# Performance work log

Hardware: AMD Instinct MI355X
Metric: run time of the kernel (lower is better)

Reference implementation:

```python
import jax, jax.numpy as jnp
from jax import lax
import numpy as np

OBJECT_W, BCE_W, DICE_W = 2.0, 5.0, 5.0
B, N, M, C = 8, 128, 32, 65536


def setup_inputs() -> dict:
    key = jax.random.key(0)
    k1, k2, k3 = jax.random.split(key, 3)
    objectness = jax.random.normal(k1, (B, N), jnp.float32)
    pred_masks = jax.random.normal(k2, (B, N, C), jnp.float32)
    gt_masks = jax.random.randint(k3, (B, M, C), 0, 2).astype(jnp.float32)
    return {"objectness": objectness, "pred_masks": pred_masks, "gt_masks": gt_masks}


def _cost_matrices(objectness, pred, gt):
    # BCE-with-logits vs all-ones target: log(1+exp(-x)) = softplus(-x)
    # BCE-with-logits vs all-zeros target: softplus(x)
    sp_pos = jax.nn.softplus(-pred)                       # [B,N,C]
    sp_neg = jax.nn.softplus(pred)                        # [B,N,C]
    # einsum('nc,mc->nm', pos, t) + einsum('nc,mc->nm', neg, 1-t), batched.
    # neg @ (1-t) = neg.sum(c) - neg @ t (avoids materializing 1-t).
    bce = (jnp.einsum('bnc,bmc->bnm', sp_pos, gt)
           + sp_neg.sum(-1)[:, :, None]
           - jnp.einsum('bnc,bmc->bnm', sp_neg, gt)) / pred.shape[-1]
    s = jax.nn.sigmoid(pred)
    numerator = 2.0 * jnp.einsum('bnc,bmc->bnm', s, gt)
    denominator = s.sum(-1)[:, :, None] + gt.sum(-1)[:, None, :]
    dice = 1.0 - (numerator + 1.0) / (denominator + 1.0)
    obj = -jax.nn.sigmoid(objectness)[:, :, None]         # [B,N,1]
    return OBJECT_W * obj + BCE_W * bce + DICE_W * dice    # [B,N,M]


def _lsap(cost):
    """Jonker-Volgenant shortest-augmenting-path LSAP (scipy algorithm).
    cost: [R, C] with R <= C. Returns col4row [R] int32: column per row."""
    R, Cn = cost.shape
    BIG = jnp.float32(1e30)

    def outer(cur_row, carry):
        u, v, row4col, col4row = carry
        shortest = jnp.full((Cn,), BIG, jnp.float32)
        path = jnp.full((Cn,), -1, jnp.int32)
        SR = jnp.zeros((R,), bool)
        SC = jnp.zeros((Cn,), bool)

        def sp_cond(s):
            return s[6] < 0

        def sp_body(s):
            i, shortest, path, SR, SC, minVal, sink = s
            SR = SR.at[i].set(True)
            d = minVal + cost[i] - u[i] - v
            better = (d < shortest) & (~SC)
            shortest = jnp.where(better, d, shortest)
            path = jnp.where(better, i, path)
            masked = jnp.where(SC, BIG, shortest)
            j = jnp.argmin(masked).astype(jnp.int32)
            minVal = masked[j]
            SC = SC.at[j].set(True)
            nxt = row4col[j]
            sink = jnp.where(nxt == -1, j, jnp.int32(-1))
            i = jnp.where(nxt == -1, i, nxt)
            return (i, shortest, path, SR, SC, minVal, sink)

        init = (cur_row.astype(jnp.int32), shortest, path, SR, SC,
                jnp.float32(0.0), jnp.int32(-1))
        i, shortest, path, SR, SC, minVal, sink = lax.while_loop(sp_cond, sp_body, init)

        # dual updates (scipy rectangular_lsap)
        u = u.at[cur_row].add(minVal)
        extra = SR & (jnp.arange(R) != cur_row)
        sp_at_col = shortest[jnp.clip(col4row, 0, Cn - 1)]
        u = jnp.where(extra, u + minVal - sp_at_col, u)
        v = jnp.where(SC, v - (minVal - shortest), v)

        # augment along path
        def aug_cond(s):
            return ~s[3]

        def aug_body(s):
            j, row4col, col4row, done = s
            i = path[j]
            row4col = row4col.at[j].set(i)
            tmp = col4row[i]
            col4row = col4row.at[i].set(j)
            done = (i == cur_row)
            return (tmp, row4col, col4row, done)

        _, row4col, col4row, _ = lax.while_loop(
            aug_cond, aug_body, (sink, row4col, col4row, jnp.array(False)))
        return (u, v, row4col, col4row)

    carry = (jnp.zeros((R,), jnp.float32), jnp.zeros((Cn,), jnp.float32),
             jnp.full((Cn,), -1, jnp.int32), jnp.full((R,), -1, jnp.int32))
    u, v, row4col, col4row = lax.fori_loop(0, R, outer, carry)
    return col4row


def reference(objectness, pred_masks, gt_masks):
    cost = _cost_matrices(objectness, pred_masks, gt_masks)   # [B,N,M]
    # scipy lsap on [N,M] then sort by target == solving on cost.T [M,N]:
    # indices[b, m] = matched query index for target m.
    indices = jax.vmap(_lsap)(jnp.transpose(cost, (0, 2, 1)))  # [B,M]
    return cost, indices
```

## Files before the change

### kernel.cpp

```cpp
#include <hip/hip_runtime.h>
#include <hip/hip_bf16.h>

#define LOG2E 1.4426950408889634f
#define LN2   0.6931471805599453f

typedef __attribute__((ext_vector_type(8))) short short8;
typedef __attribute__((ext_vector_type(4))) float f32x4;

#define B_ 8
#define N_ 128
#define M_ 32
#define C_ 65536
#define KCHUNKS 64
#define KC (C_ / KCHUNKS)
#define BK 64
#define AST 72

__device__ __forceinline__ unsigned pack2(float lo, float hi) {
  union { __hip_bfloat16 h; unsigned short s; } a, b;
  a.h = __float2bfloat16(lo);
  b.h = __float2bfloat16(hi);
  return (unsigned)a.s | ((unsigned)b.s << 16);
}

__global__ __launch_bounds__(256, 2) void cost_partial_kernel(
    const float* __restrict__ pred, const float* __restrict__ gt,
    float* __restrict__ xg_part, float* __restrict__ sg_part,
    float* __restrict__ sp_part, float* __restrict__ ss_part,
    float* __restrict__ gts_part)
{
  __shared__ unsigned short As[256 * AST];
  __shared__ unsigned short Bt[32 * AST];
  const int kc = blockIdx.x, b = blockIdx.y;
  const int tid = threadIdx.x;
  const int grp = tid >> 4, gl = tid & 15;
  const int grow = tid >> 3, gh = tid & 7;
  const int wave = tid >> 6, lane = tid & 63;
  const int quad = lane >> 4, lcol = lane & 15;
  const int c0 = kc * KC;
  const int slab = kc * B_ + b;

  const float* predB = pred + (size_t)b * N_ * C_ + c0;
  const float* gtB   = gt   + (size_t)b * M_ * C_ + (size_t)grow * C_ + c0;

  float spr[8], sr[8], gtacc = 0.f;
#pragma unroll
  for (int r = 0; r < 8; ++r) { spr[r] = 0.f; sr[r] = 0.f; }

  f32x4 acc[4][2];
#pragma unroll
  for (int rt = 0; rt < 4; ++rt)
#pragma unroll
    for (int ct = 0; ct < 2; ++ct)
      acc[rt][ct] = (f32x4){0.f, 0.f, 0.f, 0.f};

  float4 p[8], g0, g1;
#pragma unroll
  for (int r = 0; r < 8; ++r)
    p[r] = *(const float4*)(predB + (size_t)(r * 16 + grp) * C_ + gl * 4);
  g0 = *(const float4*)(gtB + gh * 4);
  g1 = *(const float4*)(gtB + (gh + 8) * 4);

  for (int ks = 0; ks < KC / BK; ++ks) {
    float4 pn[8], gn0, gn1;
    if (ks + 1 < KC / BK) {
      const int cb = (ks + 1) * BK;
#pragma unroll
      for (int r = 0; r < 8; ++r)
        pn[r] = *(const float4*)(predB + (size_t)(r * 16 + grp) * C_ + cb + gl * 4);
      gn0 = *(const float4*)(gtB + cb + gh * 4);
      gn1 = *(const float4*)(gtB + cb + (gh + 8) * 4);
    }

#pragma unroll
    for (int r = 0; r < 8; ++r) {
      const int row = r * 16 + grp;
      float xs[4] = {p[r].x, p[r].y, p[r].z, p[r].w};
      float ss[4];
#pragma unroll
      for (int e = 0; e < 4; ++e) {
        float x = xs[e];
        float t = fminf(x * LOG2E, 80.f);
        float e2 = __builtin_amdgcn_exp2f(t);
        float z = 1.f + e2;
        float s = e2 * __builtin_amdgcn_rcpf(z);
        spr[r] += __builtin_amdgcn_logf(z);
        sr[r]  += s;
        ss[e] = s;
      }
      *(uint2*)&As[row * AST + gl * 4] =
          (uint2){pack2(xs[0], xs[1]), pack2(xs[2], xs[3])};
      *(uint2*)&As[(N_ + row) * AST + gl * 4] =
          (uint2){pack2(ss[0], ss[1]), pack2(ss[2], ss[3])};
    }
    gtacc += g0.x + g0.y + g0.z + g0.w + g1.x + g1.y + g1.z + g1.w;
    *(uint2*)&Bt[grow * AST + gh * 4] =
        (uint2){pack2(g0.x, g0.y), pack2(g0.z, g0.w)};
    *(uint2*)&Bt[grow * AST + (gh + 8) * 4] =
        (uint2){pack2(g1.x, g1.y), pack2(g1.z, g1.w)};
    __syncthreads();

#pragma unroll
    for (int k0 = 0; k0 < BK; k0 += 32) {
      const int koff = k0 + quad * 8;
      short8 bf0 = *(const short8*)&Bt[lcol * AST + koff];
      short8 bf1 = *(const short8*)&Bt[(16 + lcol) * AST + koff];
#pragma unroll
      for (int rt = 0; rt < 4; ++rt) {
        short8 af = *(const short8*)&As[(wave * 64 + rt * 16 + lcol) * AST + koff];
        acc[rt][0] = __builtin_amdgcn_mfma_f32_16x16x32_bf16(af, bf0, acc[rt][0], 0, 0, 0);
        acc[rt][1] = __builtin_amdgcn_mfma_f32_16x16x32_bf16(af, bf1, acc[rt][1], 0, 0, 0);
      }
    }
    __syncthreads();

    if (ks + 1 < KC / BK) {
#pragma unroll
      for (int r = 0; r < 8; ++r) p[r] = pn[r];
      g0 = gn0; g1 = gn1;
    }
  }

#pragma unroll
  for (int r = 0; r < 8; ++r) {
    float v1 = spr[r], v2 = sr[r];
#pragma unroll
    for (int off = 1; off < 16; off <<= 1) {
      v1 += __shfl_xor(v1, off);
      v2 += __shfl_xor(v2, off);
    }
    if (gl == 0) {
      sp_part[slab * N_ + r * 16 + grp] = v1 * LN2;
      ss_part[slab * N_ + r * 16 + grp] = v2;
    }
  }
  gtacc += __shfl_xor(gtacc, 1);
  gtacc += __shfl_xor(gtacc, 2);
  gtacc += __shfl_xor(gtacc, 4);
  if (gh == 0) gts_part[slab * M_ + grow] = gtacc;

#pragma unroll
  for (int rt = 0; rt < 4; ++rt)
#pragma unroll
    for (int ct = 0; ct < 2; ++ct)
#pragma unroll
      for (int reg = 0; reg < 4; ++reg) {
        int orow = wave * 64 + rt * 16 + quad * 4 + reg;
        int ocol = ct * 16 + lcol;
        float v = acc[rt][ct][reg];
        if (orow < N_) xg_part[(slab * N_ + orow) * M_ + ocol] = v;
        else           sg_part[(slab * N_ + (orow - N_)) * M_ + ocol] = v;
      }
}

__global__ void finalize_kernel(const float* __restrict__ obj,
    const float* __restrict__ xg_part, const float* __restrict__ sg_part,
    const float* __restrict__ sp_part, const float* __restrict__ ss_part,
    const float* __restrict__ gts_part, float* __restrict__ cost)
{
  int idx = blockIdx.x * blockDim.x + threadIdx.x;
  int b = idx >> 12;
  int n = (idx >> 5) & 127;
  int m = idx & 31;
  float xa = 0.f, sa = 0.f, spa = 0.f, ssa = 0.f, ga = 0.f;
#pragma unroll 4
  for (int kc = 0; kc < KCHUNKS; ++kc) {
    int slab = kc * B_ + b;
    xa  += xg_part[(slab * N_ + n) * M_ + m];
    sa  += sg_part[(slab * N_ + n) * M_ + m];
    spa += sp_part[slab * N_ + n];
    ssa += ss_part[slab * N_ + n];
    ga  += gts_part[slab * M_ + m];
  }
  float o = obj[b * N_ + n];
  float t = fminf(o * LOG2E, 80.f);
  float e2 = __builtin_amdgcn_exp2f(t);
  float sig = e2 * __builtin_amdgcn_rcpf(1.f + e2);
  float bce = (spa - xa) * (1.0f / (float)C_);
  float dice = 1.f - (2.f * sa + 1.f) / (ssa + ga + 1.f);
  cost[idx] = -2.f * sig + 5.f * bce + 5.f * dice;
}

#define BIGF 1e30f

__device__ __forceinline__ float wave_min_all(float x) {
  const int BI = __builtin_bit_cast(int, BIGF);
  int v = __builtin_bit_cast(int, x);
#define MIN_STEP(ctrl)                                                        \
  {                                                                           \
    int t_ = __builtin_amdgcn_update_dpp(BI, v, ctrl, 0xf, 0xf, false);       \
    v = __builtin_bit_cast(int, fminf(__builtin_bit_cast(float, v),           \
                                      __builtin_bit_cast(float, t_)));        \
  }
  MIN_STEP(0x111)
  MIN_STEP(0x112)
  MIN_STEP(0x114)
  MIN_STEP(0x118)
  MIN_STEP(0x142)
  MIN_STEP(0x143)
#undef MIN_STEP
  return __builtin_bit_cast(float, __builtin_amdgcn_readlane(v, 63));
}

__device__ __forceinline__ float rdlane_f(float x, int l) {
  return __builtin_bit_cast(float, __builtin_amdgcn_readlane(__builtin_bit_cast(int, x), l));
}

__global__ __launch_bounds__(64) void lsap_kernel(const float* __restrict__ cost,
                                                  float* __restrict__ out)
{
  const int b = blockIdx.x;
  const int lane = threadIdx.x;
  __shared__ float cTs[M_ * 129];

#pragma unroll 4
  for (int t = 0; t < 16; ++t) {
    int e = t * 256 + lane * 4;
    float4 v4 = *(const float4*)&cost[b * 4096 + e];
    int n = e >> 5, m = e & 31;
    cTs[(m + 0) * 129 + n] = v4.x;
    cTs[(m + 1) * 129 + n] = v4.y;
    cTs[(m + 2) * 129 + n] = v4.z;
    cTs[(m + 3) * 129 + n] = v4.w;
  }
  __syncthreads();

  float u_reg = 0.f;
  int c4r = -1;
  float v0 = 0.f, v1 = 0.f;
  int r40 = -1, r41 = -1;

  for (int cur = 0; cur < M_; ++cur) {
    float sh0 = BIGF, sh1 = BIGF;
    int p0 = -1, p1 = -1;
    bool sc0 = false, sc1 = false;
    unsigned srmask = 0u;
    int i = cur, sink = -1;
    float minVal = 0.f;

    while (sink < 0) {
      srmask |= 1u << i;
      float ui = rdlane_f(u_reg, i);
      float cc0 = cTs[i * 129 + 2 * lane];
      float cc1 = cTs[i * 129 + 2 * lane + 1];
      float d0 = ((minVal + cc0) - ui) - v0;
      float d1 = ((minVal + cc1) - ui) - v1;
      if (!sc0 && d0 < sh0) { sh0 = d0; p0 = i; }
      if (!sc1 && d1 < sh1) { sh1 = d1; p1 = i; }
      float m0 = sc0 ? BIGF : sh0;
      float m1 = sc1 ? BIGF : sh1;
      float mv = wave_min_all(fminf(m0, m1));
      unsigned long long bl0 = __ballot(m0 == mv);
      unsigned long long bl1 = __ballot(m1 == mv);
      int j0 = bl0 ? 2 * (int)__builtin_ctzll(bl0) : 0x7fffffff;
      int j1 = bl1 ? 2 * (int)__builtin_ctzll(bl1) + 1 : 0x7fffffff;
      int j = j0 < j1 ? j0 : j1;
      minVal = mv;
      if (lane == (j >> 1)) { if (j & 1) sc1 = true; else sc0 = true; }
      int nxt = __builtin_amdgcn_readlane((j & 1) ? r41 : r40, j >> 1);
      if (nxt < 0) sink = j; else i = nxt;
    }

    int jj = c4r < 0 ? 0 : c4r;
    float g0 = __shfl(sh0, jj >> 1);
    float g1 = __shfl(sh1, jj >> 1);
    float sj = (jj & 1) ? g1 : g0;
    if (lane < M_) {
      if (lane == cur) u_reg += minVal;
      else if ((srmask >> lane) & 1u) u_reg += minVal - sj;
    }
    if (sc0) v0 -= minVal - sh0;
    if (sc1) v1 -= minVal - sh1;

    int j = sink;
    while (true) {
      int i2 = __builtin_amdgcn_readlane((j & 1) ? p1 : p0, j >> 1);
      if (lane == (j >> 1)) { if (j & 1) r41 = i2; else r40 = i2; }
      int tmp = __builtin_amdgcn_readlane(c4r, i2);
      if (lane == i2) c4r = j;
      if (i2 == cur) break;
      j = tmp;
    }
  }
  if (lane < M_) out[b * M_ + lane] = (float)c4r;
}

extern "C" void kernel_launch(void* const* d_in, const int* in_sizes, int n_in,
                              void* d_out, int out_size, void* d_ws, size_t ws_size,
                              hipStream_t stream)
{
  const float* obj  = (const float*)d_in[0];
  const float* pred = (const float*)d_in[1];
  const float* gt   = (const float*)d_in[2];
  float* out = (float*)d_out;

  float* xg_part  = (float*)d_ws;
  float* sg_part  = xg_part + (size_t)KCHUNKS * B_ * N_ * M_;
  float* sp_part  = sg_part + (size_t)KCHUNKS * B_ * N_ * M_;
  float* ss_part  = sp_part + (size_t)KCHUNKS * B_ * N_;
  float* gts_part = ss_part + (size_t)KCHUNKS * B_ * N_;

  cost_partial_kernel<<<dim3(KCHUNKS, B_), 256, 0, stream>>>(
      pred, gt, xg_part, sg_part, sp_part, ss_part, gts_part);
  finalize_kernel<<<dim3(32768 / 64), 64, 0, stream>>>(
      obj, xg_part, sg_part, sp_part, ss_part, gts_part, out);
  lsap_kernel<<<dim3(B_), 64, 0, stream>>>(out, out + 32768);
}
```

Baseline: 571.2 us.

## Load MFMA operands directly from global into registers, drop LDS staging

```diff
diff --git a/kernel.cpp b/kernel.cpp
--- a/kernel.cpp
+++ b/kernel.cpp
@@ -11,10 +11,9 @@
 #define N_ 128
 #define M_ 32
 #define C_ 65536
-#define KCHUNKS 64
+#define KCHUNKS 128
 #define KC (C_ / KCHUNKS)
-#define BK 64
-#define AST 72
+#define KSTEPS (KC / 32)
 
 __device__ __forceinline__ unsigned pack2(float lo, float hi) {
   union { __hip_bfloat16 h; unsigned short s; } a, b;
@@ -23,121 +22,144 @@
   return (unsigned)a.s | ((unsigned)b.s << 16);
 }
 
-__global__ __launch_bounds__(256, 2) void cost_partial_kernel(
+__device__ __forceinline__ short8 mk8(unsigned a, unsigned b, unsigned c, unsigned d) {
+  union { short8 v; unsigned u[4]; } r;
+  r.u[0] = a; r.u[1] = b; r.u[2] = c; r.u[3] = d;
+  return r.v;
+}
+
+__device__ __forceinline__ void actpack(float4 a, float4 bq,
+    float& spa, float& sra, short8& xf, short8& sf) {
+  float xs[8] = {a.x, a.y, a.z, a.w, bq.x, bq.y, bq.z, bq.w};
+  float sv[8];
+#pragma unroll
+  for (int e = 0; e < 8; ++e) {
+    float x = xs[e];
+    float t = fminf(x * LOG2E, 80.f);
+    float e2 = __builtin_amdgcn_exp2f(t);
+    float z = 1.f + e2;
+    float s = e2 * __builtin_amdgcn_rcpf(z);
+    spa += __builtin_amdgcn_logf(z);
+    sra += s;
+    sv[e] = s;
+  }
+  xf = mk8(pack2(xs[0], xs[1]), pack2(xs[2], xs[3]),
+           pack2(xs[4], xs[5]), pack2(xs[6], xs[7]));
+  sf = mk8(pack2(sv[0], sv[1]), pack2(sv[2], sv[3]),
+           pack2(sv[4], sv[5]), pack2(sv[6], sv[7]));
+}
+
+__device__ __forceinline__ void btpack(float4 a, float4 bq, float& ga, short8& bf) {
+  ga += a.x + a.y + a.z + a.w + bq.x + bq.y + bq.z + bq.w;
+  bf = mk8(pack2(a.x, a.y), pack2(a.z, a.w),
+           pack2(bq.x, bq.y), pack2(bq.z, bq.w));
+}
+
+__global__ __launch_bounds__(128, 2) void cost_partial_kernel(
     const float* __restrict__ pred, const float* __restrict__ gt,
     float* __restrict__ xg_part, float* __restrict__ sg_part,
     float* __restrict__ sp_part, float* __restrict__ ss_part,
     float* __restrict__ gts_part)
 {
-  __shared__ unsigned short As[256 * AST];
-  __shared__ unsigned short Bt[32 * AST];
   const int kc = blockIdx.x, b = blockIdx.y;
   const int tid = threadIdx.x;
-  const int grp = tid >> 4, gl = tid & 15;
-  const int grow = tid >> 3, gh = tid & 7;
   const int wave = tid >> 6, lane = tid & 63;
   const int quad = lane >> 4, lcol = lane & 15;
   const int c0 = kc * KC;
   const int slab = kc * B_ + b;
-
-  const float* predB = pred + (size_t)b * N_ * C_ + c0;
-  const float* gtB   = gt   + (size_t)b * M_ * C_ + (size_t)grow * C_ + c0;
-
-  float spr[8], sr[8], gtacc = 0.f;
-#pragma unroll
-  for (int r = 0; r < 8; ++r) { spr[r] = 0.f; sr[r] = 0.f; }
-
-  f32x4 acc[4][2];
+  const int wrow0 = wave * 64;
+
+  const float* pA[4];
+  const float* pB[2];
 #pragma unroll
   for (int rt = 0; rt < 4; ++rt)
+    pA[rt] = pred + ((size_t)b * N_ + wrow0 + rt * 16 + lcol) * C_ + c0 + quad * 8;
+#pragma unroll
+  for (int ct = 0; ct < 2; ++ct)
+    pB[ct] = gt + ((size_t)b * M_ + ct * 16 + lcol) * C_ + c0 + quad * 8;
+
+  f32x4 accx[4][2], accs[4][2];
+#pragma unroll
+  for (int rt = 0; rt < 4; ++rt)
+#pragma unroll
+    for (int ct = 0; ct < 2; ++ct) {
+      accx[rt][ct] = (f32x4){0.f, 0.f, 0.f, 0.f};
+      accs[rt][ct] = (f32x4){0.f, 0.f, 0.f, 0.f};
+    }
+  float spr[4] = {0.f, 0.f, 0.f, 0.f};
+  float srr[4] = {0.f, 0.f, 0.f, 0.f};
+  float gta[2] = {0.f, 0.f};
+
+  float4 a0[4], a1[4], b0[2], b1[2];
+#pragma unroll
+  for (int rt = 0; rt < 4; ++rt) {
+    a0[rt] = *(const float4*)(pA[rt]);
+    a1[rt] = *(const float4*)(pA[rt] + 4);
+  }
+#pragma unroll
+  for (int ct = 0; ct < 2; ++ct) {
+    b0[ct] = *(const float4*)(pB[ct]);
+    b1[ct] = *(const float4*)(pB[ct] + 4);
+  }
+
+  for (int kk = 0; kk < KSTEPS; ++kk) {
+    float4 na0[4], na1[4], nb0[2], nb1[2];
+    if (kk + 1 < KSTEPS) {
+      const int cb = (kk + 1) * 32;
+#pragma unroll
+      for (int rt = 0; rt < 4; ++rt) {
+        na0[rt] = *(const float4*)(pA[rt] + cb);
+        na1[rt] = *(const float4*)(pA[rt] + cb + 4);
+      }
+#pragma unroll
+      for (int ct = 0; ct < 2; ++ct) {
+        nb0[ct] = *(const float4*)(pB[ct] + cb);
+        nb1[ct] = *(const float4*)(pB[ct] + cb + 4);
+      }
+    }
+
+    short8 xf[4], sf[4], bf[2];
+#pragma unroll
+    for (int rt = 0; rt < 4; ++rt)
+      actpack(a0[rt], a1[rt], spr[rt], srr[rt], xf[rt], sf[rt]);
 #pragma unroll
     for (int ct = 0; ct < 2; ++ct)
-      acc[rt][ct] = (f32x4){0.f, 0.f, 0.f, 0.f};
-
-  float4 p[8], g0, g1;
-#pragma unroll
-  for (int r = 0; r < 8; ++r)
-    p[r] = *(const float4*)(predB + (size_t)(r * 16 + grp) * C_ + gl * 4);
-  g0 = *(const float4*)(gtB + gh * 4);
-  g1 = *(const float4*)(gtB + (gh + 8) * 4);
-
-  for (int ks = 0; ks < KC / BK; ++ks) {
-    float4 pn[8], gn0, gn1;
-    if (ks + 1 < KC / BK) {
-      const int cb = (ks + 1) * BK;
-#pragma unroll
-      for (int r = 0; r < 8; ++r)
-        pn[r] = *(const float4*)(predB + (size_t)(r * 16 + grp) * C_ + cb + gl * 4);
-      gn0 = *(const float4*)(gtB + cb + gh * 4);
-      gn1 = *(const float4*)(gtB + cb + (gh + 8) * 4);
-    }
-
-#pragma unroll
-    for (int r = 0; r < 8; ++r) {
-      const int row = r * 16 + grp;
-      float xs[4] = {p[r].x, p[r].y, p[r].z, p[r].w};
-      float ss[4];
-#pragma unroll
-      for (int e = 0; e < 4; ++e) {
-        float x = xs[e];
-        float t = fminf(x * LOG2E, 80.f);
-        float e2 = __builtin_amdgcn_exp2f(t);
-        float z = 1.f + e2;
-        float s = e2 * __builtin_amdgcn_rcpf(z);
-        spr[r] += __builtin_amdgcn_logf(z);
-        sr[r]  += s;
-        ss[e] = s;
+      btpack(b0[ct], b1[ct], gta[ct], bf[ct]);
+
+#pragma unroll
+    for (int rt = 0; rt < 4; ++rt)
+#pragma unroll
+      for (int ct = 0; ct < 2; ++ct) {
+        accx[rt][ct] = __builtin_amdgcn_mfma_f32_16x16x32_bf16(xf[rt], bf[ct], accx[rt][ct], 0, 0, 0);
+        accs[rt][ct] = __builtin_amdgcn_mfma_f32_16x16x32_bf16(sf[rt], bf[ct], accs[rt][ct], 0, 0, 0);
       }
-      *(uint2*)&As[row * AST + gl * 4] =
-          (uint2){pack2(xs[0], xs[1]), pack2(xs[2], xs[3])};
-      *(uint2*)&As[(N_ + row) * AST + gl * 4] =
-          (uint2){pack2(ss[0], ss[1]), pack2(ss[2], ss[3])};
-    }
-    gtacc += g0.x + g0.y + g0.z + g0.w + g1.x + g1.y + g1.z + g1.w;
-    *(uint2*)&Bt[grow * AST + gh * 4] =
-        (uint2){pack2(g0.x, g0.y), pack2(g0.z, g0.w)};
-    *(uint2*)&Bt[grow * AST + (gh + 8) * 4] =
-        (uint2){pack2(g1.x, g1.y), pack2(g1.z, g1.w)};
-    __syncthreads();
-
-#pragma unroll
-    for (int k0 = 0; k0 < BK; k0 += 32) {
-      const int koff = k0 + quad * 8;
-      short8 bf0 = *(const short8*)&Bt[lcol * AST + koff];
-      short8 bf1 = *(const short8*)&Bt[(16 + lcol) * AST + koff];
-#pragma unroll
-      for (int rt = 0; rt < 4; ++rt) {
-        short8 af = *(const short8*)&As[(wave * 64 + rt * 16 + lcol) * AST + koff];
-        acc[rt][0] = __builtin_amdgcn_mfma_f32_16x16x32_bf16(af, bf0, acc[rt][0], 0, 0, 0);
-        acc[rt][1] = __builtin_amdgcn_mfma_f32_16x16x32_bf16(af, bf1, acc[rt][1], 0, 0, 0);
-      }
-    }
-    __syncthreads();
-
-    if (ks + 1 < KC / BK) {
-#pragma unroll
-      for (int r = 0; r < 8; ++r) p[r] = pn[r];
-      g0 = gn0; g1 = gn1;
-    }
-  }
-
-#pragma unroll
-  for (int r = 0; r < 8; ++r) {
-    float v1 = spr[r], v2 = sr[r];
-#pragma unroll
-    for (int off = 1; off < 16; off <<= 1) {
-      v1 += __shfl_xor(v1, off);
-      v2 += __shfl_xor(v2, off);
-    }
-    if (gl == 0) {
-      sp_part[slab * N_ + r * 16 + grp] = v1 * LN2;
-      ss_part[slab * N_ + r * 16 + grp] = v2;
-    }
-  }
-  gtacc += __shfl_xor(gtacc, 1);
-  gtacc += __shfl_xor(gtacc, 2);
-  gtacc += __shfl_xor(gtacc, 4);
-  if (gh == 0) gts_part[slab * M_ + grow] = gtacc;
+
+    if (kk + 1 < KSTEPS) {
+#pragma unroll
+      for (int rt = 0; rt < 4; ++rt) { a0[rt] = na0[rt]; a1[rt] = na1[rt]; }
+#pragma unroll
+      for (int ct = 0; ct < 2; ++ct) { b0[ct] = nb0[ct]; b1[ct] = nb1[ct]; }
+    }
+  }
+
+#pragma unroll
+  for (int rt = 0; rt < 4; ++rt) {
+    float v1 = spr[rt], v2 = srr[rt];
+    v1 += __shfl_xor(v1, 16); v1 += __shfl_xor(v1, 32);
+    v2 += __shfl_xor(v2, 16); v2 += __shfl_xor(v2, 32);
+    if (quad == 0) {
+      sp_part[slab * N_ + wrow0 + rt * 16 + lcol] = v1 * LN2;
+      ss_part[slab * N_ + wrow0 + rt * 16 + lcol] = v2;
+    }
+  }
+  if (wave == 0) {
+#pragma unroll
+    for (int ct = 0; ct < 2; ++ct) {
+      float g = gta[ct];
+      g += __shfl_xor(g, 16); g += __shfl_xor(g, 32);
+      if (quad == 0) gts_part[slab * M_ + ct * 16 + lcol] = g;
+    }
+  }
 
 #pragma unroll
   for (int rt = 0; rt < 4; ++rt)
@@ -145,11 +167,10 @@
     for (int ct = 0; ct < 2; ++ct)
 #pragma unroll
       for (int reg = 0; reg < 4; ++reg) {
-        int orow = wave * 64 + rt * 16 + quad * 4 + reg;
+        int orow = wrow0 + rt * 16 + quad * 4 + reg;
         int ocol = ct * 16 + lcol;
-        float v = acc[rt][ct][reg];
-        if (orow < N_) xg_part[(slab * N_ + orow) * M_ + ocol] = v;
-        else           sg_part[(slab * N_ + (orow - N_)) * M_ + ocol] = v;
+        xg_part[((size_t)slab * N_ + orow) * M_ + ocol] = accx[rt][ct][reg];
+        sg_part[((size_t)slab * N_ + orow) * M_ + ocol] = accs[rt][ct][reg];
       }
 }
 
@@ -166,8 +187,8 @@
 #pragma unroll 4
   for (int kc = 0; kc < KCHUNKS; ++kc) {
     int slab = kc * B_ + b;
-    xa  += xg_part[(slab * N_ + n) * M_ + m];
-    sa  += sg_part[(slab * N_ + n) * M_ + m];
+    xa  += xg_part[((size_t)slab * N_ + n) * M_ + m];
+    sa  += sg_part[((size_t)slab * N_ + n) * M_ + m];
     spa += sp_part[slab * N_ + n];
     ssa += ss_part[slab * N_ + n];
     ga  += gts_part[slab * M_ + m];
@@ -300,7 +321,7 @@
   float* ss_part  = sp_part + (size_t)KCHUNKS * B_ * N_;
   float* gts_part = ss_part + (size_t)KCHUNKS * B_ * N_;
 
-  cost_partial_kernel<<<dim3(KCHUNKS, B_), 256, 0, stream>>>(
+  cost_partial_kernel<<<dim3(KCHUNKS, B_), 128, 0, stream>>>(
       pred, gt, xg_part, sg_part, sp_part, ss_part, gts_part);
   finalize_kernel<<<dim3(32768 / 64), 64, 0, stream>>>(
       obj, xg_part, sg_part, sp_part, ss_part, gts_part, out);
```

Result: no change. 570.0 us (-0.2%).

## Give each wave private LDS tiles to drop block barriers in cost GEMM

Applied to the files above, without the earlier changes.

```diff
diff --git a/kernel.cpp b/kernel.cpp
--- a/kernel.cpp
+++ b/kernel.cpp
@@ -14,6 +14,7 @@
 #define KCHUNKS 64
 #define KC (C_ / KCHUNKS)
 #define BK 64
+#define KSTEPS (KC / BK)
 #define AST 72
 
 __device__ __forceinline__ unsigned pack2(float lo, float hi) {
@@ -22,6 +23,8 @@
   b.h = __float2bfloat16(hi);
   return (unsigned)a.s | ((unsigned)b.s << 16);
 }
+
+#define MFMA16(a, bb, c) __builtin_amdgcn_mfma_f32_16x16x32_bf16(a, bb, c, 0, 0, 0)
 
 __global__ __launch_bounds__(256, 2) void cost_partial_kernel(
     const float* __restrict__ pred, const float* __restrict__ gt,
@@ -29,127 +32,132 @@
     float* __restrict__ sp_part, float* __restrict__ ss_part,
     float* __restrict__ gts_part)
 {
-  __shared__ unsigned short As[256 * AST];
-  __shared__ unsigned short Bt[32 * AST];
+  __shared__ unsigned short Xs[4][32][AST];
+  __shared__ unsigned short Ss[4][32][AST];
+  __shared__ unsigned short Gs[4][32][AST];
+
   const int kc = blockIdx.x, b = blockIdx.y;
   const int tid = threadIdx.x;
-  const int grp = tid >> 4, gl = tid & 15;
-  const int grow = tid >> 3, gh = tid & 7;
-  const int wave = tid >> 6, lane = tid & 63;
+  const int w = tid >> 6, lane = tid & 63;
   const int quad = lane >> 4, lcol = lane & 15;
   const int c0 = kc * KC;
   const int slab = kc * B_ + b;
 
-  const float* predB = pred + (size_t)b * N_ * C_ + c0;
-  const float* gtB   = gt   + (size_t)b * M_ * C_ + (size_t)grow * C_ + c0;
-
-  float spr[8], sr[8], gtacc = 0.f;
-#pragma unroll
-  for (int r = 0; r < 8; ++r) { spr[r] = 0.f; sr[r] = 0.f; }
-
-  f32x4 acc[4][2];
-#pragma unroll
-  for (int rt = 0; rt < 4; ++rt)
-#pragma unroll
-    for (int ct = 0; ct < 2; ++ct)
-      acc[rt][ct] = (f32x4){0.f, 0.f, 0.f, 0.f};
-
-  float4 p[8], g0, g1;
-#pragma unroll
-  for (int r = 0; r < 8; ++r)
-    p[r] = *(const float4*)(predB + (size_t)(r * 16 + grp) * C_ + gl * 4);
-  g0 = *(const float4*)(gtB + gh * 4);
-  g1 = *(const float4*)(gtB + (gh + 8) * 4);
-
-  for (int ks = 0; ks < KC / BK; ++ks) {
-    float4 pn[8], gn0, gn1;
-    if (ks + 1 < KC / BK) {
+  const float* pP = pred + ((size_t)(b * N_ + 32 * w + quad)) * C_ + c0 + lcol * 4;
+  const float* pG = gt   + ((size_t)(b * M_ + quad)) * C_ + c0 + lcol * 4;
+
+  f32x4 accx[2][2], accs[2][2];
+#pragma unroll
+  for (int rt = 0; rt < 2; ++rt)
+#pragma unroll
+    for (int ct = 0; ct < 2; ++ct) {
+      accx[rt][ct] = (f32x4){0.f, 0.f, 0.f, 0.f};
+      accs[rt][ct] = (f32x4){0.f, 0.f, 0.f, 0.f};
+    }
+  float spr[8], srr[8], gta[8];
+#pragma unroll
+  for (int i = 0; i < 8; ++i) { spr[i] = 0.f; srr[i] = 0.f; gta[i] = 0.f; }
+
+  float4 pc[8], gc[8];
+#pragma unroll
+  for (int i = 0; i < 8; ++i) {
+    pc[i] = *(const float4*)(pP + (size_t)(4 * i) * C_);
+    gc[i] = *(const float4*)(pG + (size_t)(4 * i) * C_);
+  }
+
+  for (int ks = 0; ks < KSTEPS; ++ks) {
+    float4 pn[8], gn[8];
+    if (ks + 1 < KSTEPS) {
       const int cb = (ks + 1) * BK;
 #pragma unroll
-      for (int r = 0; r < 8; ++r)
-        pn[r] = *(const float4*)(predB + (size_t)(r * 16 + grp) * C_ + cb + gl * 4);
-      gn0 = *(const float4*)(gtB + cb + gh * 4);
-      gn1 = *(const float4*)(gtB + cb + (gh + 8) * 4);
-    }
-
-#pragma unroll
-    for (int r = 0; r < 8; ++r) {
-      const int row = r * 16 + grp;
-      float xs[4] = {p[r].x, p[r].y, p[r].z, p[r].w};
-      float ss[4];
+      for (int i = 0; i < 8; ++i) {
+        pn[i] = *(const float4*)(pP + (size_t)(4 * i) * C_ + cb);
+        gn[i] = *(const float4*)(pG + (size_t)(4 * i) * C_ + cb);
+      }
+    }
+
+#pragma unroll
+    for (int i = 0; i < 8; ++i) {
+      const int rl = 4 * i + quad;
+      float xs[4] = {pc[i].x, pc[i].y, pc[i].z, pc[i].w};
+      float sv[4];
+      float prod = 1.f;
 #pragma unroll
       for (int e = 0; e < 4; ++e) {
-        float x = xs[e];
-        float t = fminf(x * LOG2E, 80.f);
-        float e2 = __builtin_amdgcn_exp2f(t);
+        float e2 = __builtin_amdgcn_exp2f(xs[e] * LOG2E);
         float z = 1.f + e2;
         float s = e2 * __builtin_amdgcn_rcpf(z);
-        spr[r] += __builtin_amdgcn_logf(z);
-        sr[r]  += s;
-        ss[e] = s;
+        sv[e] = s;
+        srr[i] += s;
+        prod *= z;
       }
-      *(uint2*)&As[row * AST + gl * 4] =
+      spr[i] += __builtin_amdgcn_logf(prod);
+      *(uint2*)&Xs[w][rl][lcol * 4] =
           (uint2){pack2(xs[0], xs[1]), pack2(xs[2], xs[3])};
-      *(uint2*)&As[(N_ + row) * AST + gl * 4] =
-          (uint2){pack2(ss[0], ss[1]), pack2(ss[2], ss[3])};
-    }
-    gtacc += g0.x + g0.y + g0.z + g0.w + g1.x + g1.y + g1.z + g1.w;
-    *(uint2*)&Bt[grow * AST + gh * 4] =
-        (uint2){pack2(g0.x, g0.y), pack2(g0.z, g0.w)};
-    *(uint2*)&Bt[grow * AST + (gh + 8) * 4] =
-        (uint2){pack2(g1.x, g1.y), pack2(g1.z, g1.w)};
-    __syncthreads();
-
-#pragma unroll
-    for (int k0 = 0; k0 < BK; k0 += 32) {
-      const int koff = k0 + quad * 8;
-      short8 bf0 = *(const short8*)&Bt[lcol * AST + koff];
-      short8 bf1 = *(const short8*)&Bt[(16 + lcol) * AST + koff];
-#pragma unroll
-      for (int rt = 0; rt < 4; ++rt) {
-        short8 af = *(const short8*)&As[(wave * 64 + rt * 16 + lcol) * AST + koff];
-        acc[rt][0] = __builtin_amdgcn_mfma_f32_16x16x32_bf16(af, bf0, acc[rt][0], 0, 0, 0);
-        acc[rt][1] = __builtin_amdgcn_mfma_f32_16x16x32_bf16(af, bf1, acc[rt][1], 0, 0, 0);
+      *(uint2*)&Ss[w][rl][lcol * 4] =
+          (uint2){pack2(sv[0], sv[1]), pack2(sv[2], sv[3])};
+      float4 gv = gc[i];
+      if (w == 0) gta[i] += gv.x + gv.y + gv.z + gv.w;
+      *(uint2*)&Gs[w][rl][lcol * 4] =
+          (uint2){pack2(gv.x, gv.y), pack2(gv.z, gv.w)};
+    }
+
+#pragma unroll
+    for (int kh = 0; kh < 2; ++kh) {
+      const int ko = kh * 32 + quad * 8;
+      short8 bf0 = *(const short8*)&Gs[w][lcol][ko];
+      short8 bf1 = *(const short8*)&Gs[w][16 + lcol][ko];
+#pragma unroll
+      for (int rt = 0; rt < 2; ++rt) {
+        short8 xf = *(const short8*)&Xs[w][16 * rt + lcol][ko];
+        short8 sf = *(const short8*)&Ss[w][16 * rt + lcol][ko];
+        accx[rt][0] = MFMA16(xf, bf0, accx[rt][0]);
+        accx[rt][1] = MFMA16(xf, bf1, accx[rt][1]);
+        accs[rt][0] = MFMA16(sf, bf0, accs[rt][0]);
+        accs[rt][1] = MFMA16(sf, bf1, accs[rt][1]);
       }
     }
-    __syncthreads();
-
-    if (ks + 1 < KC / BK) {
-#pragma unroll
-      for (int r = 0; r < 8; ++r) p[r] = pn[r];
-      g0 = gn0; g1 = gn1;
-    }
-  }
-
-#pragma unroll
-  for (int r = 0; r < 8; ++r) {
-    float v1 = spr[r], v2 = sr[r];
+
+    if (ks + 1 < KSTEPS) {
+#pragma unroll
+      for (int i = 0; i < 8; ++i) { pc[i] = pn[i]; gc[i] = gn[i]; }
+    }
+  }
+
+#pragma unroll
+  for (int i = 0; i < 8; ++i) {
+    float v1 = spr[i], v2 = srr[i];
 #pragma unroll
     for (int off = 1; off < 16; off <<= 1) {
       v1 += __shfl_xor(v1, off);
       v2 += __shfl_xor(v2, off);
     }
-    if (gl == 0) {
-      sp_part[slab * N_ + r * 16 + grp] = v1 * LN2;
-      ss_part[slab * N_ + r * 16 + grp] = v2;
-    }
-  }
-  gtacc += __shfl_xor(gtacc, 1);
-  gtacc += __shfl_xor(gtacc, 2);
-  gtacc += __shfl_xor(gtacc, 4);
-  if (gh == 0) gts_part[slab * M_ + grow] = gtacc;
-
-#pragma unroll
-  for (int rt = 0; rt < 4; ++rt)
+    if (lcol == 0) {
+      int row = 32 * w + 4 * i + quad;
+      sp_part[slab * N_ + row] = v1 * LN2;
+      ss_part[slab * N_ + row] = v2;
+    }
+  }
+  if (w == 0) {
+#pragma unroll
+    for (int i = 0; i < 8; ++i) {
+      float gv = gta[i];
+#pragma unroll
+      for (int off = 1; off < 16; off <<= 1) gv += __shfl_xor(gv, off);
+      if (lcol == 0) gts_part[slab * M_ + 4 * i + quad] = gv;
+    }
+  }
+
+#pragma unroll
+  for (int rt = 0; rt < 2; ++rt)
 #pragma unroll
     for (int ct = 0; ct < 2; ++ct)
 #pragma unroll
       for (int reg = 0; reg < 4; ++reg) {
-        int orow = wave * 64 + rt * 16 + quad * 4 + reg;
-        int ocol = ct * 16 + lcol;
-        float v = acc[rt][ct][reg];
-        if (orow < N_) xg_part[(slab * N_ + orow) * M_ + ocol] = v;
-        else           sg_part[(slab * N_ + (orow - N_)) * M_ + ocol] = v;
+        int n = 32 * w + 16 * rt + quad * 4 + reg;
+        int m = 16 * ct + lcol;
+        xg_part[((size_t)slab * N_ + n) * M_ + m] = accx[rt][ct][reg];
+        sg_part[((size_t)slab * N_ + n) * M_ + m] = accs[rt][ct][reg];
       }
 }
 
@@ -166,15 +174,14 @@
 #pragma unroll 4
   for (int kc = 0; kc < KCHUNKS; ++kc) {
     int slab = kc * B_ + b;
-    xa  += xg_part[(slab * N_ + n) * M_ + m];
-    sa  += sg_part[(slab * N_ + n) * M_ + m];
+    xa  += xg_part[((size_t)slab * N_ + n) * M_ + m];
+    sa  += sg_part[((size_t)slab * N_ + n) * M_ + m];
     spa += sp_part[slab * N_ + n];
     ssa += ss_part[slab * N_ + n];
     ga  += gts_part[slab * M_ + m];
   }
   float o = obj[b * N_ + n];
-  float t = fminf(o * LOG2E, 80.f);
-  float e2 = __builtin_amdgcn_exp2f(t);
+  float e2 = __builtin_amdgcn_exp2f(o * LOG2E);
   float sig = e2 * __builtin_amdgcn_rcpf(1.f + e2);
   float bce = (spa - xa) * (1.0f / (float)C_);
   float dice = 1.f - (2.f * sa + 1.f) / (ssa + ga + 1.f);
@@ -302,7 +309,7 @@
 
   cost_partial_kernel<<<dim3(KCHUNKS, B_), 256, 0, stream>>>(
       pred, gt, xg_part, sg_part, sp_part, ss_part, gts_part);
-  finalize_kernel<<<dim3(32768 / 64), 64, 0, stream>>>(
+  finalize_kernel<<<dim3(32768 / 128), 128, 0, stream>>>(
       obj, xg_part, sg_part, sp_part, ss_part, gts_part, out);
   lsap_kernel<<<dim3(B_), 64, 0, stream>>>(out, out + 32768);
 }
```

New measurement: 584.7 us. +2.4%, slower.
